# Optimization experiments

Measured on AMD Instinct MI355X. Metric: run time of the kernel, lower is better.

Reference implementation:

```python
import jax, jax.numpy as jnp
import numpy as np

TOL = 1e-7  # tolerant_zero_error
HID = 32


def _gcn_layer(x, a, W, b):
    # spektral-style GCNConv: relu(A_norm @ X @ W + b)
    return jax.nn.relu(jnp.einsum('bnm,bmf->bnf', a, x @ W) + b)


def setup_inputs() -> dict:
    key = jax.random.key(0)
    ks = jax.random.split(key, 12)
    B, N, F = 8, 2048, 64
    x = jax.random.normal(ks[0], (B, N, F), dtype=jnp.float32)
    a = jax.random.uniform(ks[1], (B, N, N), dtype=jnp.float32)
    def he(k, shape):
        fan_in = shape[0]
        lim = jnp.sqrt(6.0 / fan_in)
        return jax.random.uniform(k, shape, jnp.float32, -lim, lim)
    return {
        'x': x, 'a': a,
        'W1': he(ks[2], (F, HID)),   'b1': jnp.zeros((HID,), jnp.float32),
        'W2': he(ks[3], (HID, HID)), 'b2': jnp.zeros((HID,), jnp.float32),
        'W3': he(ks[4], (HID, HID)), 'b3': jnp.zeros((HID,), jnp.float32),
        'Wf1': he(ks[5], (HID, 2 * HID)), 'bf1': jnp.zeros((2 * HID,), jnp.float32),
        'Wf2': he(ks[6], (2 * HID, 1)),   'bf2': jnp.zeros((1,), jnp.float32),
    }


def reference(x, a, W1, b1, W2, b2, W3, b3, Wf1, bf1, Wf2, bf2):
    x = x.astype(jnp.float32)
    a = a.astype(jnp.float32)
    B, N, _ = a.shape
    # add_self_loop: put 1 on diagonal entries whose current value is ~0
    diag = jnp.diagonal(a, axis1=-2, axis2=-1)            # [B,N]
    add = jnp.where(jnp.abs(diag) < TOL, 1.0, 0.0)        # [B,N]
    eye = jnp.eye(N, dtype=a.dtype)
    a = a + add[:, :, None] * eye
    # norm_a: D^-1/2 A D^-1/2 (diag matmuls == elementwise d_i * a_ij * d_j)
    d = jnp.sum(a, axis=-1)                               # [B,N]
    dm = d ** -0.5
    a = dm[:, :, None] * a * dm[:, None, :]
    # GCNConv stack
    h = _gcn_layer(x, a, W1, b1)
    h = _gcn_layer(h, a, W2, b2)
    h = _gcn_layer(h, a, W3, b3)
    # GlobalMaxPool over nodes
    g = jnp.max(h, axis=1)                                # [B,HID]
    # MLP head
    g = jax.nn.relu(g @ Wf1 + bf1)
    out = g @ Wf2 + bf2                                   # [B,1]
    return out
```

## Files before the change

kernel.cpp:

```cpp
#include <hip/hip_runtime.h>

#define BB 8
#define NN 2048
#define FF 64
#define HH 32

typedef __attribute__((ext_vector_type(8))) short short8;
typedef __attribute__((ext_vector_type(4))) float floatx4;

static __device__ __forceinline__ float warp_sum64(float v) {
  for (int off = 32; off; off >>= 1) v += __shfl_down(v, off, 64);
  return v;
}

static __device__ __forceinline__ unsigned int f2bf_rne(float f) {
  unsigned int u = __float_as_uint(f);
  return (u + 0x7fffu + ((u >> 16) & 1u)) >> 16;
}
static __device__ __forceinline__ float bf2f(unsigned short s) {
  return __uint_as_float(((unsigned int)s) << 16);
}

#define GLOAD_LDS16(g, l)                                                 \
  __builtin_amdgcn_global_load_lds(                                       \
      (const __attribute__((address_space(1))) unsigned int*)(g),         \
      (__attribute__((address_space(3))) unsigned int*)(l), 16, 0, 0)

__global__ __launch_bounds__(256) void deg_cvt_kernel(const float* __restrict__ A,
                                                      float* __restrict__ dm,
                                                      float* __restrict__ addf,
                                                      unsigned short* __restrict__ Abf) {
  const int lane = threadIdx.x & 63;
  const int w = threadIdx.x >> 6;
  const size_t row = (size_t)blockIdx.x * 4 + w;
  const size_t n = row & (NN - 1);
  const float* Ar = A + row * (size_t)NN;
  unsigned int* Abr = (unsigned int*)(Abf + row * (size_t)NN);
  float sum = 0.f;
#pragma unroll
  for (int it = 0; it < 8; ++it) {
    float4 v = *(const float4*)(Ar + it * 256 + lane * 4);
    sum += v.x + v.y + v.z + v.w;
    uint2 p;
    p.x = f2bf_rne(v.x) | (f2bf_rne(v.y) << 16);
    p.y = f2bf_rne(v.z) | (f2bf_rne(v.w) << 16);
    *(uint2*)(Abr + it * 128 + lane * 2) = p;
  }
  sum = warp_sum64(sum);
  if (lane == 0) {
    const float diag = Ar[n];
    const float ad = (fabsf(diag) < 1e-7f) ? 1.f : 0.f;
    dm[row] = 1.f / sqrtf(sum + ad);
    addf[row] = ad;
  }
}

__global__ __launch_bounds__(256) void xw_kernel(const float* __restrict__ x,
                                                 const float* __restrict__ W1,
                                                 const float* __restrict__ dm,
                                                 unsigned short* __restrict__ hst) {
  __shared__ float xs[8][FF + 1];
  __shared__ float wl[FF * HH];
  const int tid = threadIdx.x;
  const size_t row0 = (size_t)blockIdx.x * 8;
  for (int k = tid; k < FF * HH; k += 256) wl[k] = W1[k];
  for (int k = tid; k < 8 * FF; k += 256) xs[k >> 6][k & 63] = x[row0 * FF + k];
  __syncthreads();
  const int r = tid >> 5, c = tid & 31;
  float acc = 0.f;
#pragma unroll
  for (int k = 0; k < FF; ++k) acc = fmaf(xs[r][k], wl[k * HH + c], acc);
  const size_t row = row0 + r;
  const int b = (int)(row >> 11);
  const int n = (int)(row & (NN - 1));
  hst[((size_t)b * HH + c) * NN + n] = (unsigned short)f2bf_rne(dm[row] * acc);
}

__global__ __launch_bounds__(256) void layer_kernel(const unsigned short* __restrict__ Abf,
                                                    const unsigned short* __restrict__ hst_in,
                                                    const float* __restrict__ dm,
                                                    const float* __restrict__ addf,
                                                    const float* __restrict__ bias,
                                                    const float* __restrict__ Wn,
                                                    unsigned short* __restrict__ hst_next,
                                                    unsigned int* __restrict__ gmax,
                                                    const int do_pool) {
  __shared__ unsigned char Asm[2][8192];
  __shared__ unsigned char Bsm[2][8192];
  __shared__ float wl[HH * HH];
  __shared__ float hbuf[32][HH + 1];
  __shared__ float pbuf[8][HH];

  const int tid = threadIdx.x;
  const int mb = blockIdx.x & 63;
  const int b = blockIdx.x >> 6;
  const int mrow0 = mb * 32;
  const int lane = tid & 63;
  const int w = tid >> 6;
  const int mt = w >> 1, nt = w & 1;

  if (!do_pool)
    for (int k = tid; k < HH * HH; k += 256) wl[k] = Wn[k];

  const int r0 = tid >> 4;
  const int gd = tid & 15;
  const int gs = (gd & 8) | ((gd & 7) ^ (r0 & 7));
  const unsigned short* aSrc0 =
      Abf + ((size_t)(b * NN + mrow0 + r0) * NN) + gs * 8;
  const unsigned short* bSrc0 =
      hst_in + ((size_t)(b * HH + r0) * NN) + gs * 8;
  const int waveBase = (tid >> 6) * 1024;

  const int q = lane >> 4;
  const int arow = mt * 16 + (lane & 15);
  const int nrow = nt * 16 + (lane & 15);
  int aoff[4], boff[4];
#pragma unroll
  for (int ks = 0; ks < 4; ++ks) {
    const int g = ks * 4 + q;
    aoff[ks] = arow * 256 + (((g & 8) | ((g & 7) ^ (arow & 7))) * 16);
    boff[ks] = nrow * 256 + (((g & 8) | ((g & 7) ^ (nrow & 7))) * 16);
  }

  floatx4 acc = {0.f, 0.f, 0.f, 0.f};

#define STAGE(k0, p)                                                     \
  do {                                                                   \
    GLOAD_LDS16(aSrc0 + (k0), &Asm[p][waveBase]);                        \
    GLOAD_LDS16(aSrc0 + (k0) + 16 * (size_t)NN, &Asm[p][4096 + waveBase]); \
    GLOAD_LDS16(bSrc0 + (k0), &Bsm[p][waveBase]);                        \
    GLOAD_LDS16(bSrc0 + (k0) + 16 * (size_t)NN, &Bsm[p][4096 + waveBase]); \
  } while (0)

  STAGE(0, 0);
#pragma unroll 4
  for (int c = 0; c < 16; ++c) {
    __syncthreads();
    if (c + 1 < 16) STAGE((c + 1) * 128, (c + 1) & 1);
    const unsigned char* Ab = Asm[c & 1];
    const unsigned char* Bb = Bsm[c & 1];
#pragma unroll
    for (int ks = 0; ks < 4; ++ks) {
      short8 af = *(const short8*)(Ab + aoff[ks]);
      short8 bf = *(const short8*)(Bb + boff[ks]);
      acc = __builtin_amdgcn_mfma_f32_16x16x32_bf16(af, bf, acc, 0, 0, 0);
    }
  }

  const int colc = nt * 16 + (lane & 15);
  __syncthreads();
#pragma unroll
  for (int r = 0; r < 4; ++r) {
    const int rowb = mt * 16 + q * 4 + r;
    const int rg = b * NN + mrow0 + rowb;
    const float hsin = bf2f(hst_in[((size_t)b * HH + colc) * NN + mrow0 + rowb]);
    const float h = fmaf(dm[rg], acc[r] + addf[rg] * hsin, bias[colc]);
    hbuf[rowb][colc] = fmaxf(h, 0.f);
  }
  __syncthreads();

  const int col = tid & 31;
  const int rq = tid >> 5;
  if (do_pool) {
    float m = hbuf[rq * 4][col];
#pragma unroll
    for (int i = 1; i < 4; ++i) m = fmaxf(m, hbuf[rq * 4 + i][col]);
    pbuf[rq][col] = m;
    __syncthreads();
    if (tid < HH) {
      float mm = pbuf[0][tid];
#pragma unroll
      for (int r = 1; r < 8; ++r) mm = fmaxf(mm, pbuf[r][tid]);
      atomicMax(&gmax[b * HH + tid], __float_as_uint(mm));
    }
  } else {
    unsigned short outv[4];
#pragma unroll
    for (int i = 0; i < 4; ++i) {
      const int row = rq * 4 + i;
      const int rg = b * NN + mrow0 + row;
      float acc2 = 0.f;
#pragma unroll
      for (int k = 0; k < HH; ++k)
        acc2 = fmaf(hbuf[row][k], wl[k * HH + col], acc2);
      outv[i] = (unsigned short)f2bf_rne(dm[rg] * acc2);
    }
    *(ushort4*)(hst_next + ((size_t)b * HH + col) * NN + mrow0 + rq * 4) =
        *(ushort4*)outv;
  }
#undef STAGE
}

__global__ __launch_bounds__(64) void head_kernel(const unsigned int* __restrict__ gmax,
                                                  const float* __restrict__ Wf1,
                                                  const float* __restrict__ bf1,
                                                  const float* __restrict__ Wf2,
                                                  const float* __restrict__ bf2,
                                                  float* __restrict__ out) {
  const int b = blockIdx.x;
  const int t = threadIdx.x;
  float acc = bf1[t];
#pragma unroll
  for (int c = 0; c < HH; ++c)
    acc = fmaf(__uint_as_float(gmax[b * HH + c]), Wf1[c * (2 * HH) + t], acc);
  acc = fmaxf(acc, 0.f);
  float v = acc * Wf2[t];
  v = warp_sum64(v);
  if (t == 0) out[b] = v + bf2[0];
}

extern "C" void kernel_launch(void* const* d_in, const int* in_sizes, int n_in,
                              void* d_out, int out_size, void* d_ws, size_t ws_size,
                              hipStream_t stream) {
  const float* x   = (const float*)d_in[0];
  const float* a   = (const float*)d_in[1];
  const float* W1  = (const float*)d_in[2];
  const float* b1  = (const float*)d_in[3];
  const float* W2  = (const float*)d_in[4];
  const float* b2  = (const float*)d_in[5];
  const float* W3  = (const float*)d_in[6];
  const float* b3  = (const float*)d_in[7];
  const float* Wf1 = (const float*)d_in[8];
  const float* bf1 = (const float*)d_in[9];
  const float* Wf2 = (const float*)d_in[10];
  const float* bf2 = (const float*)d_in[11];
  float* out = (float*)d_out;

  float* ws = (float*)d_ws;
  const size_t BN = (size_t)BB * NN;
  float* dm   = ws;
  float* addf = dm + BN;
  unsigned int* gmax = (unsigned int*)(addf + BN);
  unsigned short* hst_a = (unsigned short*)(gmax + 256);
  unsigned short* hst_b = hst_a + BN * HH;
  unsigned short* Abf = hst_b + BN * HH;

  hipMemsetAsync(gmax, 0, BB * HH * sizeof(unsigned int), stream);

  deg_cvt_kernel<<<BN / 4, 256, 0, stream>>>(a, dm, addf, Abf);
  xw_kernel<<<BN / 8, 256, 0, stream>>>(x, W1, dm, hst_a);

  layer_kernel<<<BB * 64, 256, 0, stream>>>(Abf, hst_a, dm, addf, b1, W2, hst_b, nullptr, 0);
  layer_kernel<<<BB * 64, 256, 0, stream>>>(Abf, hst_b, dm, addf, b2, W3, hst_a, nullptr, 0);
  layer_kernel<<<BB * 64, 256, 0, stream>>>(Abf, hst_a, dm, addf, b3, nullptr, nullptr, gmax, 1);

  head_kernel<<<BB, 64, 0, stream>>>(gmax, Wf1, bf1, Wf2, bf2, out);
}
```

Measured before the change: 291.0 us.

## Restructure GCN layer kernel into single-wave blocks with triple-buffered async loads

The layer kernel now runs one 64-thread wave per block covering 16 rows and all 32 hidden columns, with two MFMA accumulators. Loads from global memory into LDS use a three-stage ring buffer synchronized by explicit vmcnt waits in place of block barriers, and the pooling reduction uses wave shuffles. The aim is to remove __syncthreads overhead, deepen prefetch, and double the block count for better latency hiding. In exchange, every block reloads the full hidden tile, so total hidden-state traffic doubles, and the W matrix is read straight from global memory during the epilogue instead of from LDS.

```diff
diff --git a/kernel.cpp b/kernel.cpp
--- a/kernel.cpp
+++ b/kernel.cpp
@@ -4,6 +4,8 @@
 #define NN 2048
 #define FF 64
 #define HH 32
+#define CK 128
+#define NCHK (NN / CK)
 
 typedef __attribute__((ext_vector_type(8))) short short8;
 typedef __attribute__((ext_vector_type(4))) float floatx4;
@@ -76,119 +78,134 @@
   hst[((size_t)b * HH + c) * NN + n] = (unsigned short)f2bf_rne(dm[row] * acc);
 }
 
-__global__ __launch_bounds__(256) void layer_kernel(const unsigned short* __restrict__ Abf,
-                                                    const unsigned short* __restrict__ hst_in,
-                                                    const float* __restrict__ dm,
-                                                    const float* __restrict__ addf,
-                                                    const float* __restrict__ bias,
-                                                    const float* __restrict__ Wn,
-                                                    unsigned short* __restrict__ hst_next,
-                                                    unsigned int* __restrict__ gmax,
-                                                    const int do_pool) {
-  __shared__ unsigned char Asm[2][8192];
-  __shared__ unsigned char Bsm[2][8192];
-  __shared__ float wl[HH * HH];
-  __shared__ float hbuf[32][HH + 1];
-  __shared__ float pbuf[8][HH];
+__global__ __launch_bounds__(64) void layer_kernel(const unsigned short* __restrict__ Abf,
+                                                   const unsigned short* __restrict__ hst_in,
+                                                   const float* __restrict__ dm,
+                                                   const float* __restrict__ addf,
+                                                   const float* __restrict__ bias,
+                                                   const float* __restrict__ Wn,
+                                                   unsigned short* __restrict__ hst_next,
+                                                   unsigned int* __restrict__ gmax,
+                                                   const int do_pool) {
+  __shared__ __align__(16) unsigned char smem[3][12288];
 
   const int tid = threadIdx.x;
-  const int mb = blockIdx.x & 63;
-  const int b = blockIdx.x >> 6;
-  const int mrow0 = mb * 32;
-  const int lane = tid & 63;
-  const int w = tid >> 6;
-  const int mt = w >> 1, nt = w & 1;
-
-  if (!do_pool)
-    for (int k = tid; k < HH * HH; k += 256) wl[k] = Wn[k];
-
-  const int r0 = tid >> 4;
-  const int gd = tid & 15;
-  const int gs = (gd & 8) | ((gd & 7) ^ (r0 & 7));
-  const unsigned short* aSrc0 =
-      Abf + ((size_t)(b * NN + mrow0 + r0) * NN) + gs * 8;
-  const unsigned short* bSrc0 =
-      hst_in + ((size_t)(b * HH + r0) * NN) + gs * 8;
-  const int waveBase = (tid >> 6) * 1024;
-
-  const int q = lane >> 4;
-  const int arow = mt * 16 + (lane & 15);
-  const int nrow = nt * 16 + (lane & 15);
-  int aoff[4], boff[4];
-#pragma unroll
-  for (int ks = 0; ks < 4; ++ks) {
-    const int g = ks * 4 + q;
-    aoff[ks] = arow * 256 + (((g & 8) | ((g & 7) ^ (arow & 7))) * 16);
-    boff[ks] = nrow * 256 + (((g & 8) | ((g & 7) ^ (nrow & 7))) * 16);
-  }
-
-  floatx4 acc = {0.f, 0.f, 0.f, 0.f};
-
-#define STAGE(k0, p)                                                     \
-  do {                                                                   \
-    GLOAD_LDS16(aSrc0 + (k0), &Asm[p][waveBase]);                        \
-    GLOAD_LDS16(aSrc0 + (k0) + 16 * (size_t)NN, &Asm[p][4096 + waveBase]); \
-    GLOAD_LDS16(bSrc0 + (k0), &Bsm[p][waveBase]);                        \
-    GLOAD_LDS16(bSrc0 + (k0) + 16 * (size_t)NN, &Bsm[p][4096 + waveBase]); \
+  const int mb = blockIdx.x & 127;
+  const int b = blockIdx.x >> 7;
+  const int mrow0 = mb * 16;
+  const int q = tid >> 4;
+  const int l15 = tid & 15;
+
+  const unsigned short* aSrc[4];
+  const unsigned short* bSrc[8];
+#pragma unroll
+  for (int i = 0; i < 4; ++i) {
+    const int r = i * 4 + q;
+    const int gl = l15 ^ r;
+    aSrc[i] = Abf + ((size_t)(b * NN + mrow0 + r)) * NN + gl * 8;
+  }
+#pragma unroll
+  for (int i = 0; i < 8; ++i) {
+    const int r = i * 4 + q;
+    const int gl = l15 ^ (r & 15);
+    bSrc[i] = hst_in + ((size_t)(b * HH + r)) * NN + gl * 8;
+  }
+
+#define ISSUE(buf)                                                        \
+  do {                                                                    \
+    _Pragma("unroll") for (int i = 0; i < 4; ++i) {                       \
+      GLOAD_LDS16(aSrc[i], &smem[buf][i * 1024]);                         \
+      aSrc[i] += CK;                                                      \
+    }                                                                     \
+    _Pragma("unroll") for (int i = 0; i < 8; ++i) {                       \
+      GLOAD_LDS16(bSrc[i], &smem[buf][4096 + i * 1024]);                  \
+      bSrc[i] += CK;                                                      \
+    }                                                                     \
   } while (0)
 
-  STAGE(0, 0);
-#pragma unroll 4
-  for (int c = 0; c < 16; ++c) {
+  floatx4 acc0 = {0.f, 0.f, 0.f, 0.f};
+  floatx4 acc1 = {0.f, 0.f, 0.f, 0.f};
+
+  ISSUE(0);
+  ISSUE(1);
+#pragma unroll
+  for (int c = 0; c < NCHK; ++c) {
+    if (c + 2 < NCHK) ISSUE((c + 2) % 3);
+    if (c <= NCHK - 3) {
+      asm volatile("s_waitcnt vmcnt(24)" ::: "memory");
+    } else if (c == NCHK - 2) {
+      asm volatile("s_waitcnt vmcnt(12)" ::: "memory");
+    } else {
+      asm volatile("s_waitcnt vmcnt(0)" ::: "memory");
+    }
+    const unsigned char* Ab = smem[c % 3];
+    const unsigned char* Bb = smem[c % 3] + 4096;
+#pragma unroll
+    for (int ks = 0; ks < 4; ++ks) {
+      const int go = (((ks * 4 + q) ^ l15) * 16);
+      short8 af = *(const short8*)(Ab + l15 * 256 + go);
+      short8 b0 = *(const short8*)(Bb + l15 * 256 + go);
+      short8 b1 = *(const short8*)(Bb + 4096 + l15 * 256 + go);
+      acc0 = __builtin_amdgcn_mfma_f32_16x16x32_bf16(af, b0, acc0, 0, 0, 0);
+      acc1 = __builtin_amdgcn_mfma_f32_16x16x32_bf16(af, b1, acc1, 0, 0, 0);
+    }
+  }
+#undef ISSUE
+
+  float h0[4], h1[4];
+#pragma unroll
+  for (int r = 0; r < 4; ++r) {
+    const int row = q * 4 + r;
+    const int rg = b * NN + mrow0 + row;
+    const float dmv = dm[rg], adv = addf[rg];
+    const float hs0 = bf2f(hst_in[((size_t)b * HH + l15) * NN + mrow0 + row]);
+    const float hs1 = bf2f(hst_in[((size_t)b * HH + 16 + l15) * NN + mrow0 + row]);
+    h0[r] = fmaxf(fmaf(dmv, acc0[r] + adv * hs0, bias[l15]), 0.f);
+    h1[r] = fmaxf(fmaf(dmv, acc1[r] + adv * hs1, bias[16 + l15]), 0.f);
+  }
+
+  if (do_pool) {
+    float m0 = fmaxf(fmaxf(h0[0], h0[1]), fmaxf(h0[2], h0[3]));
+    float m1 = fmaxf(fmaxf(h1[0], h1[1]), fmaxf(h1[2], h1[3]));
+    m0 = fmaxf(m0, __shfl_xor(m0, 16, 64));
+    m0 = fmaxf(m0, __shfl_xor(m0, 32, 64));
+    m1 = fmaxf(m1, __shfl_xor(m1, 16, 64));
+    m1 = fmaxf(m1, __shfl_xor(m1, 32, 64));
+    if (q == 0) {
+      atomicMax(&gmax[b * HH + l15], __float_as_uint(m0));
+      atomicMax(&gmax[b * HH + 16 + l15], __float_as_uint(m1));
+    }
+  } else {
+    float* hb = (float*)&smem[0][0];
     __syncthreads();
-    if (c + 1 < 16) STAGE((c + 1) * 128, (c + 1) & 1);
-    const unsigned char* Ab = Asm[c & 1];
-    const unsigned char* Bb = Bsm[c & 1];
-#pragma unroll
-    for (int ks = 0; ks < 4; ++ks) {
-      short8 af = *(const short8*)(Ab + aoff[ks]);
-      short8 bf = *(const short8*)(Bb + boff[ks]);
-      acc = __builtin_amdgcn_mfma_f32_16x16x32_bf16(af, bf, acc, 0, 0, 0);
-    }
-  }
-
-  const int colc = nt * 16 + (lane & 15);
-  __syncthreads();
-#pragma unroll
-  for (int r = 0; r < 4; ++r) {
-    const int rowb = mt * 16 + q * 4 + r;
-    const int rg = b * NN + mrow0 + rowb;
-    const float hsin = bf2f(hst_in[((size_t)b * HH + colc) * NN + mrow0 + rowb]);
-    const float h = fmaf(dm[rg], acc[r] + addf[rg] * hsin, bias[colc]);
-    hbuf[rowb][colc] = fmaxf(h, 0.f);
-  }
-  __syncthreads();
-
-  const int col = tid & 31;
-  const int rq = tid >> 5;
-  if (do_pool) {
-    float m = hbuf[rq * 4][col];
-#pragma unroll
-    for (int i = 1; i < 4; ++i) m = fmaxf(m, hbuf[rq * 4 + i][col]);
-    pbuf[rq][col] = m;
+#pragma unroll
+    for (int r = 0; r < 4; ++r) {
+      const int row = q * 4 + r;
+      hb[row * 33 + l15] = h0[r];
+      hb[row * 33 + 16 + l15] = h1[r];
+    }
     __syncthreads();
-    if (tid < HH) {
-      float mm = pbuf[0][tid];
-#pragma unroll
-      for (int r = 1; r < 8; ++r) mm = fmaxf(mm, pbuf[r][tid]);
-      atomicMax(&gmax[b * HH + tid], __float_as_uint(mm));
-    }
-  } else {
-    unsigned short outv[4];
-#pragma unroll
-    for (int i = 0; i < 4; ++i) {
-      const int row = rq * 4 + i;
+    unsigned short o0[4], o1[4];
+#pragma unroll
+    for (int r = 0; r < 4; ++r) {
+      const int row = q * 4 + r;
       const int rg = b * NN + mrow0 + row;
-      float acc2 = 0.f;
-#pragma unroll
-      for (int k = 0; k < HH; ++k)
-        acc2 = fmaf(hbuf[row][k], wl[k * HH + col], acc2);
-      outv[i] = (unsigned short)f2bf_rne(dm[rg] * acc2);
-    }
-    *(ushort4*)(hst_next + ((size_t)b * HH + col) * NN + mrow0 + rq * 4) =
-        *(ushort4*)outv;
-  }
-#undef STAGE
+      float s0 = 0.f, s1 = 0.f;
+#pragma unroll
+      for (int k = 0; k < HH; ++k) {
+        const float hv = hb[row * 33 + k];
+        s0 = fmaf(hv, Wn[k * HH + l15], s0);
+        s1 = fmaf(hv, Wn[k * HH + 16 + l15], s1);
+      }
+      const float dmv = dm[rg];
+      o0[r] = (unsigned short)f2bf_rne(dmv * s0);
+      o1[r] = (unsigned short)f2bf_rne(dmv * s1);
+    }
+    *(ushort4*)(hst_next + ((size_t)b * HH + l15) * NN + mrow0 + q * 4) =
+        *(ushort4*)o0;
+    *(ushort4*)(hst_next + ((size_t)b * HH + 16 + l15) * NN + mrow0 + q * 4) =
+        *(ushort4*)o1;
+  }
 }
 
 __global__ __launch_bounds__(64) void head_kernel(const unsigned int* __restrict__ gmax,
@@ -240,9 +257,9 @@
   deg_cvt_kernel<<<BN / 4, 256, 0, stream>>>(a, dm, addf, Abf);
   xw_kernel<<<BN / 8, 256, 0, stream>>>(x, W1, dm, hst_a);
 
-  layer_kernel<<<BB * 64, 256, 0, stream>>>(Abf, hst_a, dm, addf, b1, W2, hst_b, nullptr, 0);
-  layer_kernel<<<BB * 64, 256, 0, stream>>>(Abf, hst_b, dm, addf, b2, W3, hst_a, nullptr, 0);
-  layer_kernel<<<BB * 64, 256, 0, stream>>>(Abf, hst_a, dm, addf, b3, nullptr, nullptr, gmax, 1);
+  layer_kernel<<<BB * 128, 64, 0, stream>>>(Abf, hst_a, dm, addf, b1, W2, hst_b, nullptr, 0);
+  layer_kernel<<<BB * 128, 64, 0, stream>>>(Abf, hst_b, dm, addf, b2, W3, hst_a, nullptr, 0);
+  layer_kernel<<<BB * 128, 64, 0, stream>>>(Abf, hst_a, dm, addf, b3, nullptr, nullptr, gmax, 1);
 
   head_kernel<<<BB, 64, 0, stream>>>(gmax, Wf1, bf1, Wf2, bf2, out);
 }
```

New measurement: 278.1 us. -4.5%, faster.

## Replace direct global-to-LDS loads with register-staged double-buffered prefetch and padded LDS rows

Applied to the files above, without the earlier changes.

The layer GEMM's staging changes from global_load_lds 16-byte async copies into XOR-swizzled LDS to ordinary vector loads into registers, prefetched two chunks ahead and then written into a padded LDS layout (272-byte rows). A and B tiles now share one buffer per stage, and the loop is fully unrolled. The aim is to hide global latency with a deeper register prefetch and to avoid bank conflicts through padding instead of swizzling. In exchange it uses more registers and LDS traffic, and the LDS stores now sit on each iteration's critical path before the barrier.

```diff
diff --git a/kernel.cpp b/kernel.cpp
--- a/kernel.cpp
+++ b/kernel.cpp
@@ -4,6 +4,9 @@
 #define NN 2048
 #define FF 64
 #define HH 32
+#define CK 128
+#define NCHK (NN / CK)
+#define ROWB 272
 
 typedef __attribute__((ext_vector_type(8))) short short8;
 typedef __attribute__((ext_vector_type(4))) float floatx4;
@@ -20,11 +23,6 @@
 static __device__ __forceinline__ float bf2f(unsigned short s) {
   return __uint_as_float(((unsigned int)s) << 16);
 }
-
-#define GLOAD_LDS16(g, l)                                                 \
-  __builtin_amdgcn_global_load_lds(                                       \
-      (const __attribute__((address_space(1))) unsigned int*)(g),         \
-      (__attribute__((address_space(3))) unsigned int*)(l), 16, 0, 0)
 
 __global__ __launch_bounds__(256) void deg_cvt_kernel(const float* __restrict__ A,
                                                       float* __restrict__ dm,
@@ -85,8 +83,7 @@
                                                     unsigned short* __restrict__ hst_next,
                                                     unsigned int* __restrict__ gmax,
                                                     const int do_pool) {
-  __shared__ unsigned char Asm[2][8192];
-  __shared__ unsigned char Bsm[2][8192];
+  __shared__ __align__(16) unsigned char sbuf[2][64 * ROWB];
   __shared__ float wl[HH * HH];
   __shared__ float hbuf[32][HH + 1];
   __shared__ float pbuf[8][HH];
@@ -102,52 +99,55 @@
   if (!do_pool)
     for (int k = tid; k < HH * HH; k += 256) wl[k] = Wn[k];
 
-  const int r0 = tid >> 4;
-  const int gd = tid & 15;
-  const int gs = (gd & 8) | ((gd & 7) ^ (r0 & 7));
-  const unsigned short* aSrc0 =
-      Abf + ((size_t)(b * NN + mrow0 + r0) * NN) + gs * 8;
-  const unsigned short* bSrc0 =
-      hst_in + ((size_t)(b * HH + r0) * NN) + gs * 8;
-  const int waveBase = (tid >> 6) * 1024;
+  const int ra = tid >> 3;
+  const int g0 = tid & 7;
+  const unsigned short* __restrict__ aS =
+      Abf + ((size_t)(b * NN + mrow0 + ra)) * NN + g0 * 8;
+  const unsigned short* __restrict__ bS =
+      hst_in + ((size_t)(b * HH + ra)) * NN + g0 * 8;
+  const int adst0 = ra * ROWB + g0 * 16;
+  const int adst1 = ra * ROWB + (8 + g0) * 16;
+  const int bdst0 = (32 + ra) * ROWB + g0 * 16;
+  const int bdst1 = (32 + ra) * ROWB + (8 + g0) * 16;
 
   const int q = lane >> 4;
-  const int arow = mt * 16 + (lane & 15);
-  const int nrow = nt * 16 + (lane & 15);
-  int aoff[4], boff[4];
-#pragma unroll
-  for (int ks = 0; ks < 4; ++ks) {
-    const int g = ks * 4 + q;
-    aoff[ks] = arow * 256 + (((g & 8) | ((g & 7) ^ (arow & 7))) * 16);
-    boff[ks] = nrow * 256 + (((g & 8) | ((g & 7) ^ (nrow & 7))) * 16);
-  }
+  const int l15 = lane & 15;
+  const int arow = mt * 16 + l15;
+  const int brow = 32 + nt * 16 + l15;
 
   floatx4 acc = {0.f, 0.f, 0.f, 0.f};
 
-#define STAGE(k0, p)                                                     \
-  do {                                                                   \
-    GLOAD_LDS16(aSrc0 + (k0), &Asm[p][waveBase]);                        \
-    GLOAD_LDS16(aSrc0 + (k0) + 16 * (size_t)NN, &Asm[p][4096 + waveBase]); \
-    GLOAD_LDS16(bSrc0 + (k0), &Bsm[p][waveBase]);                        \
-    GLOAD_LDS16(bSrc0 + (k0) + 16 * (size_t)NN, &Bsm[p][4096 + waveBase]); \
+  uint4 rA0[2], rA1[2], rB0[2], rB1[2];
+#define GLOAD(p, kc)                                  \
+  do {                                                \
+    rA0[p] = *(const uint4*)(aS + (kc));              \
+    rA1[p] = *(const uint4*)(aS + (kc) + 64);         \
+    rB0[p] = *(const uint4*)(bS + (kc));              \
+    rB1[p] = *(const uint4*)(bS + (kc) + 64);         \
   } while (0)
 
-  STAGE(0, 0);
-#pragma unroll 4
-  for (int c = 0; c < 16; ++c) {
+  GLOAD(0, 0);
+  GLOAD(1, CK);
+#pragma unroll
+  for (int c = 0; c < NCHK; ++c) {
+    const int p = c & 1;
+    *(uint4*)(&sbuf[p][adst0]) = rA0[p];
+    *(uint4*)(&sbuf[p][adst1]) = rA1[p];
+    *(uint4*)(&sbuf[p][bdst0]) = rB0[p];
+    *(uint4*)(&sbuf[p][bdst1]) = rB1[p];
     __syncthreads();
-    if (c + 1 < 16) STAGE((c + 1) * 128, (c + 1) & 1);
-    const unsigned char* Ab = Asm[c & 1];
-    const unsigned char* Bb = Bsm[c & 1];
-#pragma unroll
-    for (int ks = 0; ks < 4; ++ks) {
-      short8 af = *(const short8*)(Ab + aoff[ks]);
-      short8 bf = *(const short8*)(Bb + boff[ks]);
+    if (c + 2 < NCHK) GLOAD(p, (c + 2) * CK);
+    const unsigned char* base = sbuf[p];
+#pragma unroll
+    for (int s = 0; s < 4; ++s) {
+      short8 af = *(const short8*)(base + arow * ROWB + s * 64 + q * 16);
+      short8 bf = *(const short8*)(base + brow * ROWB + s * 64 + q * 16);
       acc = __builtin_amdgcn_mfma_f32_16x16x32_bf16(af, bf, acc, 0, 0, 0);
     }
   }
-
-  const int colc = nt * 16 + (lane & 15);
+#undef GLOAD
+
+  const int colc = nt * 16 + l15;
   __syncthreads();
 #pragma unroll
   for (int r = 0; r < 4; ++r) {
@@ -188,7 +188,6 @@
     *(ushort4*)(hst_next + ((size_t)b * HH + col) * NN + mrow0 + rq * 4) =
         *(ushort4*)outv;
   }
-#undef STAGE
 }
 
 __global__ __launch_bounds__(64) void head_kernel(const unsigned int* __restrict__ gmax,
```

New measurement: 375.4 us. 29.0% more time.
